# Kernel optimization log

Hardware: AMD Instinct MI355X
Metric: run time of the kernel (lower is better)

The kernel has to match this reference:

```python
import jax, jax.numpy as jnp
import numpy as np

ALPHA = 1.0

def _phi(x):
    # ELU(alpha)+1 feature map
    return jax.nn.elu(x, alpha=ALPHA) + 1.0

def setup_inputs() -> dict:
    key = jax.random.key(0)
    kq, kk, kv = jax.random.split(key, 3)
    B, H, N, D = 8, 8, 1024, 64
    Q = jax.random.normal(kq, (B, H, N, D), dtype=jnp.float32)
    K = jax.random.normal(kk, (B, H, N, D), dtype=jnp.float32)
    # NOTE: original torch code divides [.,N,dv] by [.,N,N] elementwise, so dv must equal N
    V = jax.random.normal(kv, (B, H, N, N), dtype=jnp.float32)
    return {"Q": Q, "K": K, "V": V}

def reference(Q, K, V):
    # denominator: phi(Q) @ phi(K)^T -> [B,H,N,N]
    denominator = jnp.einsum('bhnd,bhmd->bhnm', _phi(Q), _phi(K))
    # numerator: denominator @ V -> [B,H,N,N] (since dv == N)
    numerator = jnp.einsum('bhnm,bhmv->bhnv', denominator, V)
    return numerator / denominator
```

## Files before the change

kernel.cpp:

```cpp
#include <hip/hip_runtime.h>
#include <math.h>

typedef __attribute__((ext_vector_type(8))) short bf16x8;
typedef __attribute__((ext_vector_type(4))) float f32x4;
typedef __attribute__((ext_vector_type(4))) float float4v;
typedef __attribute__((ext_vector_type(2))) float float2v;
typedef __attribute__((ext_vector_type(4))) unsigned short ushort4v;

#define N_TOK 1024
#define D_DIM 64
#define BMt 128
#define BNt 128
#define BKt 32
#define KP 72
#define SP 40

__device__ __forceinline__ unsigned short f2bf(float f) {
    union { float f; unsigned u; } v; v.f = f;
    return (unsigned short)((v.u + 0x7fffu + ((v.u >> 16) & 1u)) >> 16);
}
__device__ __forceinline__ float bf2f(unsigned short h) {
    union { unsigned u; float f; } v; v.u = ((unsigned)h) << 16;
    return v.f;
}
__device__ __forceinline__ float phif(float x) {
    return x > 0.0f ? x + 1.0f : __expf(x);
}

__global__ __launch_bounds__(256)
void ka_fused(const float* __restrict__ Qp, const float* __restrict__ Kp,
              const float* __restrict__ Vp, float* __restrict__ Op)
{
    __shared__ unsigned short KhiS[32][KP], KloS[32][KP];
    __shared__ unsigned short VthiS[128][SP], VtloS[128][SP];
    __shared__ unsigned short ShiS[128][SP], SloS[128][SP];

    const int tid  = threadIdx.x;
    const int lane = tid & 63;
    const int wid  = tid >> 6;
    const int wr   = wid >> 1;
    const int wc   = wid & 1;
    const int lr   = lane & 15;
    const int lg   = lane >> 4;
    const int j0   = blockIdx.x * BNt;
    const int i0   = blockIdx.y * BMt;
    const int bh   = blockIdx.z;

    const size_t qkbase = (size_t)bh * N_TOK * D_DIM;
    const size_t vbase  = (size_t)bh * N_TOK * N_TOK;

    const f32x4 fzero = {0.f, 0.f, 0.f, 0.f};

    bf16x8 qhi[2][2], qlo[2][2];
    #pragma unroll
    for (int fr = 0; fr < 2; ++fr) {
        #pragma unroll
        for (int kb = 0; kb < 2; ++kb) {
            const float* src = Qp + qkbase
                + (size_t)(i0 + wid * 32 + fr * 16 + lr) * D_DIM + kb * 32 + lg * 8;
            float4v a = *(const float4v*)src;
            float4v b = *(const float4v*)(src + 4);
            float x[8] = {a[0], a[1], a[2], a[3], b[0], b[1], b[2], b[3]};
            bf16x8 h, l;
            #pragma unroll
            for (int e = 0; e < 8; ++e) {
                float p = phif(x[e]);
                unsigned short hh = f2bf(p);
                h[e] = (short)hh;
                l[e] = (short)f2bf(p - bf2f(hh));
            }
            qhi[fr][kb] = h;
            qlo[fr][kb] = l;
        }
    }

    f32x4 acc[4][4];
    #pragma unroll
    for (int a = 0; a < 4; ++a)
        #pragma unroll
        for (int b = 0; b < 4; ++b)
            acc[a][b] = fzero;

    for (int ms = 0; ms < N_TOK / BKt; ++ms) {
        const int m0 = ms * BKt;
        __syncthreads();

        #pragma unroll
        for (int r2 = 0; r2 < 2; ++r2) {
            int f   = tid + r2 * 256;
            int row = f >> 4;
            int dq  = (f & 15) * 4;
            float4v v = *(const float4v*)(Kp + qkbase + (size_t)(m0 + row) * D_DIM + dq);
            ushort4v h, l;
            #pragma unroll
            for (int e = 0; e < 4; ++e) {
                float p = phif(v[e]);
                h[e] = f2bf(p);
                l[e] = f2bf(p - bf2f(h[e]));
            }
            *(ushort4v*)&KhiS[row][dq] = h;
            *(ushort4v*)&KloS[row][dq] = l;
        }

        {
            int c2 = tid & 63;
            int mh = tid >> 6;
            int n  = 2 * c2;
            float va[8], vb[8];
            #pragma unroll
            for (int r = 0; r < 8; ++r) {
                float2v t = *(const float2v*)(Vp + vbase
                    + (size_t)(m0 + mh * 8 + r) * N_TOK + j0 + n);
                va[r] = t[0];
                vb[r] = t[1];
            }
            bf16x8 h, l;
            #pragma unroll
            for (int e = 0; e < 8; ++e) {
                unsigned short hh = f2bf(va[e]);
                h[e] = (short)hh;
                l[e] = (short)f2bf(va[e] - bf2f(hh));
            }
            *(bf16x8*)&VthiS[n][mh * 8] = h;
            *(bf16x8*)&VtloS[n][mh * 8] = l;
            #pragma unroll
            for (int e = 0; e < 8; ++e) {
                unsigned short hh = f2bf(vb[e]);
                h[e] = (short)hh;
                l[e] = (short)f2bf(vb[e] - bf2f(hh));
            }
            *(bf16x8*)&VthiS[n + 1][mh * 8] = h;
            *(bf16x8*)&VtloS[n + 1][mh * 8] = l;
        }
        __syncthreads();

        #pragma unroll
        for (int fr = 0; fr < 2; ++fr) {
            #pragma unroll
            for (int fc = 0; fc < 2; ++fc) {
                f32x4 sa = fzero;
                #pragma unroll
                for (int kb = 0; kb < 2; ++kb) {
                    int mcol = fc * 16 + lr;
                    int d0   = kb * 32 + lg * 8;
                    bf16x8 kh = *(const bf16x8*)&KhiS[mcol][d0];
                    bf16x8 kl = *(const bf16x8*)&KloS[mcol][d0];
                    sa = __builtin_amdgcn_mfma_f32_16x16x32_bf16(qhi[fr][kb], kh, sa, 0, 0, 0);
                    sa = __builtin_amdgcn_mfma_f32_16x16x32_bf16(qhi[fr][kb], kl, sa, 0, 0, 0);
                    sa = __builtin_amdgcn_mfma_f32_16x16x32_bf16(qlo[fr][kb], kh, sa, 0, 0, 0);
                }
                int col = fc * 16 + lr;
                int r0  = wid * 32 + fr * 16 + lg * 4;
                #pragma unroll
                for (int r = 0; r < 4; ++r) {
                    unsigned short hh = f2bf(sa[r]);
                    ShiS[r0 + r][col] = hh;
                    SloS[r0 + r][col] = f2bf(sa[r] - bf2f(hh));
                }
            }
        }
        __syncthreads();

        {
            bf16x8 sh[4], sl[4];
            int k0 = lg * 8;
            #pragma unroll
            for (int am = 0; am < 4; ++am) {
                int row = wr * 64 + am * 16 + lr;
                sh[am] = *(const bf16x8*)&ShiS[row][k0];
                sl[am] = *(const bf16x8*)&SloS[row][k0];
            }
            #pragma unroll
            for (int bn = 0; bn < 4; ++bn) {
                int col = wc * 64 + bn * 16 + lr;
                bf16x8 vh = *(const bf16x8*)&VthiS[col][k0];
                bf16x8 vl = *(const bf16x8*)&VtloS[col][k0];
                #pragma unroll
                for (int am = 0; am < 4; ++am) {
                    acc[am][bn] = __builtin_amdgcn_mfma_f32_16x16x32_bf16(sh[am], vh, acc[am][bn], 0, 0, 0);
                    acc[am][bn] = __builtin_amdgcn_mfma_f32_16x16x32_bf16(sh[am], vl, acc[am][bn], 0, 0, 0);
                    acc[am][bn] = __builtin_amdgcn_mfma_f32_16x16x32_bf16(sl[am], vh, acc[am][bn], 0, 0, 0);
                }
            }
        }
    }

    #pragma unroll
    for (int ch = 0; ch < 4; ++ch) {
        __syncthreads();
        #pragma unroll
        for (int r2 = 0; r2 < 2; ++r2) {
            int f   = tid + r2 * 256;
            int row = f >> 4;
            int dq  = (f & 15) * 4;
            float4v v = *(const float4v*)(Kp + qkbase
                + (size_t)(j0 + ch * 32 + row) * D_DIM + dq);
            ushort4v h, l;
            #pragma unroll
            for (int e = 0; e < 4; ++e) {
                float p = phif(v[e]);
                h[e] = f2bf(p);
                l[e] = f2bf(p - bf2f(h[e]));
            }
            *(ushort4v*)&KhiS[row][dq] = h;
            *(ushort4v*)&KloS[row][dq] = l;
        }
        __syncthreads();

        if (wc == (ch >> 1)) {
            const int bp = ch & 1;
            #pragma unroll
            for (int am = 0; am < 4; ++am) {
                bf16x8 qh2[2], ql2[2];
                #pragma unroll
                for (int kb = 0; kb < 2; ++kb) {
                    const float* src = Qp + qkbase
                        + (size_t)(i0 + wr * 64 + am * 16 + lr) * D_DIM + kb * 32 + lg * 8;
                    float4v a = *(const float4v*)src;
                    float4v b = *(const float4v*)(src + 4);
                    float x[8] = {a[0], a[1], a[2], a[3], b[0], b[1], b[2], b[3]};
                    bf16x8 h, l;
                    #pragma unroll
                    for (int e = 0; e < 8; ++e) {
                        float p = phif(x[e]);
                        unsigned short hh = f2bf(p);
                        h[e] = (short)hh;
                        l[e] = (short)f2bf(p - bf2f(hh));
                    }
                    qh2[kb] = h;
                    ql2[kb] = l;
                }
                #pragma unroll
                for (int fc = 0; fc < 2; ++fc) {
                    f32x4 da = fzero;
                    #pragma unroll
                    for (int kb = 0; kb < 2; ++kb) {
                        int mcol = fc * 16 + lr;
                        int d0   = kb * 32 + lg * 8;
                        bf16x8 kh = *(const bf16x8*)&KhiS[mcol][d0];
                        bf16x8 kl = *(const bf16x8*)&KloS[mcol][d0];
                        da = __builtin_amdgcn_mfma_f32_16x16x32_bf16(qh2[kb], kh, da, 0, 0, 0);
                        da = __builtin_amdgcn_mfma_f32_16x16x32_bf16(qh2[kb], kl, da, 0, 0, 0);
                        da = __builtin_amdgcn_mfma_f32_16x16x32_bf16(ql2[kb], kh, da, 0, 0, 0);
                    }
                    const int bn    = bp * 2 + fc;
                    int ocol  = j0 + wc * 64 + bn * 16 + lr;
                    int orow0 = i0 + wr * 64 + am * 16 + lg * 4;
                    #pragma unroll
                    for (int r = 0; r < 4; ++r) {
                        Op[(size_t)bh * N_TOK * N_TOK + (size_t)(orow0 + r) * N_TOK + ocol] =
                            acc[am][bn][r] / da[r];
                    }
                }
            }
        }
    }
}

extern "C" void kernel_launch(void* const* d_in, const int* in_sizes, int n_in,
                              void* d_out, int out_size, void* d_ws, size_t ws_size,
                              hipStream_t stream)
{
    const float* Q = (const float*)d_in[0];
    const float* K = (const float*)d_in[1];
    const float* V = (const float*)d_in[2];
    float* O = (float*)d_out;
    dim3 grid(N_TOK / BNt, N_TOK / BMt, 8 * 8);
    ka_fused<<<grid, 256, 0, stream>>>(Q, K, V, O);
}
```

Measured before the change: 1.291 ms.

## Drop split-bf16 low parts for phi(Q), phi(K) and V; keep split only for S

Replaces the three-term split-bf16 emulation with single bf16 for phi(Q), phi(K) and V, keeping the hi/lo split only for the intermediate S tile. This cuts MFMA count (S and denominator from 3 to 1 per k-step, PV from 3 to 2), halves LDS for K and V^T, and swaps the conversion to cheaper round-half-up packing via v_perm. It also transposes the QK^T MFMA operand order so S is written with vector stores, and remaps V load threads. The trade-off is lower accuracy in the numerator and denominator, which may exceed tolerance.

```diff
diff --git a/kernel.cpp b/kernel.cpp
--- a/kernel.cpp
+++ b/kernel.cpp
@@ -5,7 +5,8 @@
 typedef __attribute__((ext_vector_type(4))) float f32x4;
 typedef __attribute__((ext_vector_type(4))) float float4v;
 typedef __attribute__((ext_vector_type(2))) float float2v;
-typedef __attribute__((ext_vector_type(4))) unsigned short ushort4v;
+typedef __attribute__((ext_vector_type(2))) unsigned uint2v;
+typedef __attribute__((ext_vector_type(4))) unsigned uint4v;
 
 #define N_TOK 1024
 #define D_DIM 64
@@ -15,24 +16,25 @@
 #define KP 72
 #define SP 40
 
-__device__ __forceinline__ unsigned short f2bf(float f) {
-    union { float f; unsigned u; } v; v.f = f;
-    return (unsigned short)((v.u + 0x7fffu + ((v.u >> 16) & 1u)) >> 16);
-}
-__device__ __forceinline__ float bf2f(unsigned short h) {
-    union { unsigned u; float f; } v; v.u = ((unsigned)h) << 16;
-    return v.f;
-}
 __device__ __forceinline__ float phif(float x) {
     return x > 0.0f ? x + 1.0f : __expf(x);
+}
+__device__ __forceinline__ unsigned pk2(float a, float b) {
+    unsigned ua = __builtin_bit_cast(unsigned, a) + 0x8000u;
+    unsigned ub = __builtin_bit_cast(unsigned, b) + 0x8000u;
+    return __builtin_amdgcn_perm(ub, ua, 0x07060302u);
+}
+__device__ __forceinline__ unsigned pk2t(float a, float b) {
+    return __builtin_amdgcn_perm(__builtin_bit_cast(unsigned, b),
+                                 __builtin_bit_cast(unsigned, a), 0x07060302u);
 }
 
 __global__ __launch_bounds__(256)
 void ka_fused(const float* __restrict__ Qp, const float* __restrict__ Kp,
               const float* __restrict__ Vp, float* __restrict__ Op)
 {
-    __shared__ unsigned short KhiS[32][KP], KloS[32][KP];
-    __shared__ unsigned short VthiS[128][SP], VtloS[128][SP];
+    __shared__ unsigned short KhS[32][KP];
+    __shared__ unsigned short VtS[128][SP];
     __shared__ unsigned short ShiS[128][SP], SloS[128][SP];
 
     const int tid  = threadIdx.x;
@@ -48,29 +50,20 @@
 
     const size_t qkbase = (size_t)bh * N_TOK * D_DIM;
     const size_t vbase  = (size_t)bh * N_TOK * N_TOK;
-
     const f32x4 fzero = {0.f, 0.f, 0.f, 0.f};
 
-    bf16x8 qhi[2][2], qlo[2][2];
+    bf16x8 qh[2][2];
     #pragma unroll
-    for (int fr = 0; fr < 2; ++fr) {
+    for (int fc = 0; fc < 2; ++fc) {
         #pragma unroll
         for (int kb = 0; kb < 2; ++kb) {
             const float* src = Qp + qkbase
-                + (size_t)(i0 + wid * 32 + fr * 16 + lr) * D_DIM + kb * 32 + lg * 8;
+                + (size_t)(i0 + wid * 32 + fc * 16 + lr) * D_DIM + kb * 32 + lg * 8;
             float4v a = *(const float4v*)src;
             float4v b = *(const float4v*)(src + 4);
-            float x[8] = {a[0], a[1], a[2], a[3], b[0], b[1], b[2], b[3]};
-            bf16x8 h, l;
-            #pragma unroll
-            for (int e = 0; e < 8; ++e) {
-                float p = phif(x[e]);
-                unsigned short hh = f2bf(p);
-                h[e] = (short)hh;
-                l[e] = (short)f2bf(p - bf2f(hh));
-            }
-            qhi[fr][kb] = h;
-            qlo[fr][kb] = l;
+            uint4v w = { pk2(phif(a[0]), phif(a[1])), pk2(phif(a[2]), phif(a[3])),
+                         pk2(phif(b[0]), phif(b[1])), pk2(phif(b[2]), phif(b[3])) };
+            qh[fc][kb] = __builtin_bit_cast(bf16x8, w);
         }
     }
 
@@ -91,46 +84,24 @@
             int row = f >> 4;
             int dq  = (f & 15) * 4;
             float4v v = *(const float4v*)(Kp + qkbase + (size_t)(m0 + row) * D_DIM + dq);
-            ushort4v h, l;
-            #pragma unroll
-            for (int e = 0; e < 4; ++e) {
-                float p = phif(v[e]);
-                h[e] = f2bf(p);
-                l[e] = f2bf(p - bf2f(h[e]));
-            }
-            *(ushort4v*)&KhiS[row][dq] = h;
-            *(ushort4v*)&KloS[row][dq] = l;
+            uint2v w = { pk2(phif(v[0]), phif(v[1])), pk2(phif(v[2]), phif(v[3])) };
+            *(uint2v*)&KhS[row][dq] = w;
         }
 
         {
-            int c2 = tid & 63;
-            int mh = tid >> 6;
-            int n  = 2 * c2;
+            const int mh = tid & 3;
+            const int c2 = tid >> 2;
+            const float* vsrc = Vp + vbase + (size_t)(m0 + mh * 8) * N_TOK + j0 + 2 * c2;
             float va[8], vb[8];
             #pragma unroll
             for (int r = 0; r < 8; ++r) {
-                float2v t = *(const float2v*)(Vp + vbase
-                    + (size_t)(m0 + mh * 8 + r) * N_TOK + j0 + n);
-                va[r] = t[0];
-                vb[r] = t[1];
-            }
-            bf16x8 h, l;
-            #pragma unroll
-            for (int e = 0; e < 8; ++e) {
-                unsigned short hh = f2bf(va[e]);
-                h[e] = (short)hh;
-                l[e] = (short)f2bf(va[e] - bf2f(hh));
-            }
-            *(bf16x8*)&VthiS[n][mh * 8] = h;
-            *(bf16x8*)&VtloS[n][mh * 8] = l;
-            #pragma unroll
-            for (int e = 0; e < 8; ++e) {
-                unsigned short hh = f2bf(vb[e]);
-                h[e] = (short)hh;
-                l[e] = (short)f2bf(vb[e] - bf2f(hh));
-            }
-            *(bf16x8*)&VthiS[n + 1][mh * 8] = h;
-            *(bf16x8*)&VtloS[n + 1][mh * 8] = l;
+                float2v t = *(const float2v*)(vsrc + (size_t)r * N_TOK);
+                va[r] = t[0]; vb[r] = t[1];
+            }
+            uint4v wa = { pk2(va[0], va[1]), pk2(va[2], va[3]), pk2(va[4], va[5]), pk2(va[6], va[7]) };
+            uint4v wb = { pk2(vb[0], vb[1]), pk2(vb[2], vb[3]), pk2(vb[4], vb[5]), pk2(vb[6], vb[7]) };
+            *(uint4v*)&VtS[2 * c2][mh * 8]     = wa;
+            *(uint4v*)&VtS[2 * c2 + 1][mh * 8] = wb;
         }
         __syncthreads();
 
@@ -141,29 +112,31 @@
                 f32x4 sa = fzero;
                 #pragma unroll
                 for (int kb = 0; kb < 2; ++kb) {
-                    int mcol = fc * 16 + lr;
-                    int d0   = kb * 32 + lg * 8;
-                    bf16x8 kh = *(const bf16x8*)&KhiS[mcol][d0];
-                    bf16x8 kl = *(const bf16x8*)&KloS[mcol][d0];
-                    sa = __builtin_amdgcn_mfma_f32_16x16x32_bf16(qhi[fr][kb], kh, sa, 0, 0, 0);
-                    sa = __builtin_amdgcn_mfma_f32_16x16x32_bf16(qhi[fr][kb], kl, sa, 0, 0, 0);
-                    sa = __builtin_amdgcn_mfma_f32_16x16x32_bf16(qlo[fr][kb], kh, sa, 0, 0, 0);
-                }
-                int col = fc * 16 + lr;
-                int r0  = wid * 32 + fr * 16 + lg * 4;
-                #pragma unroll
-                for (int r = 0; r < 4; ++r) {
-                    unsigned short hh = f2bf(sa[r]);
-                    ShiS[r0 + r][col] = hh;
-                    SloS[r0 + r][col] = f2bf(sa[r] - bf2f(hh));
-                }
+                    bf16x8 ka = *(const bf16x8*)&KhS[fr * 16 + lr][kb * 32 + lg * 8];
+                    sa = __builtin_amdgcn_mfma_f32_16x16x32_bf16(ka, qh[fc][kb], sa, 0, 0, 0);
+                }
+                unsigned t0 = __builtin_bit_cast(unsigned, sa[0]) + 0x8000u;
+                unsigned t1 = __builtin_bit_cast(unsigned, sa[1]) + 0x8000u;
+                unsigned t2 = __builtin_bit_cast(unsigned, sa[2]) + 0x8000u;
+                unsigned t3 = __builtin_bit_cast(unsigned, sa[3]) + 0x8000u;
+                uint2v hv = { __builtin_amdgcn_perm(t1, t0, 0x07060302u),
+                              __builtin_amdgcn_perm(t3, t2, 0x07060302u) };
+                float l0 = sa[0] - __builtin_bit_cast(float, t0 & 0xffff0000u);
+                float l1 = sa[1] - __builtin_bit_cast(float, t1 & 0xffff0000u);
+                float l2 = sa[2] - __builtin_bit_cast(float, t2 & 0xffff0000u);
+                float l3 = sa[3] - __builtin_bit_cast(float, t3 & 0xffff0000u);
+                uint2v lv = { pk2t(l0, l1), pk2t(l2, l3) };
+                const int irow = wid * 32 + fc * 16 + lr;
+                const int mcol = fr * 16 + lg * 4;
+                *(uint2v*)&ShiS[irow][mcol] = hv;
+                *(uint2v*)&SloS[irow][mcol] = lv;
             }
         }
         __syncthreads();
 
         {
+            const int k0 = lg * 8;
             bf16x8 sh[4], sl[4];
-            int k0 = lg * 8;
             #pragma unroll
             for (int am = 0; am < 4; ++am) {
                 int row = wr * 64 + am * 16 + lr;
@@ -173,12 +146,10 @@
             #pragma unroll
             for (int bn = 0; bn < 4; ++bn) {
                 int col = wc * 64 + bn * 16 + lr;
-                bf16x8 vh = *(const bf16x8*)&VthiS[col][k0];
-                bf16x8 vl = *(const bf16x8*)&VtloS[col][k0];
+                bf16x8 vh = *(const bf16x8*)&VtS[col][k0];
                 #pragma unroll
                 for (int am = 0; am < 4; ++am) {
                     acc[am][bn] = __builtin_amdgcn_mfma_f32_16x16x32_bf16(sh[am], vh, acc[am][bn], 0, 0, 0);
-                    acc[am][bn] = __builtin_amdgcn_mfma_f32_16x16x32_bf16(sh[am], vl, acc[am][bn], 0, 0, 0);
                     acc[am][bn] = __builtin_amdgcn_mfma_f32_16x16x32_bf16(sl[am], vh, acc[am][bn], 0, 0, 0);
                 }
             }
@@ -195,15 +166,8 @@
             int dq  = (f & 15) * 4;
             float4v v = *(const float4v*)(Kp + qkbase
                 + (size_t)(j0 + ch * 32 + row) * D_DIM + dq);
-            ushort4v h, l;
-            #pragma unroll
-            for (int e = 0; e < 4; ++e) {
-                float p = phif(v[e]);
-                h[e] = f2bf(p);
-                l[e] = f2bf(p - bf2f(h[e]));
-            }
-            *(ushort4v*)&KhiS[row][dq] = h;
-            *(ushort4v*)&KloS[row][dq] = l;
+            uint2v w = { pk2(phif(v[0]), phif(v[1])), pk2(phif(v[2]), phif(v[3])) };
+            *(uint2v*)&KhS[row][dq] = w;
         }
         __syncthreads();
 
@@ -211,41 +175,28 @@
             const int bp = ch & 1;
             #pragma unroll
             for (int am = 0; am < 4; ++am) {
-                bf16x8 qh2[2], ql2[2];
+                bf16x8 qa[2];
                 #pragma unroll
                 for (int kb = 0; kb < 2; ++kb) {
                     const float* src = Qp + qkbase
                         + (size_t)(i0 + wr * 64 + am * 16 + lr) * D_DIM + kb * 32 + lg * 8;
                     float4v a = *(const float4v*)src;
                     float4v b = *(const float4v*)(src + 4);
-                    float x[8] = {a[0], a[1], a[2], a[3], b[0], b[1], b[2], b[3]};
-                    bf16x8 h, l;
-                    #pragma unroll
-                    for (int e = 0; e < 8; ++e) {
-                        float p = phif(x[e]);
-                        unsigned short hh = f2bf(p);
-                        h[e] = (short)hh;
-                        l[e] = (short)f2bf(p - bf2f(hh));
-                    }
-                    qh2[kb] = h;
-                    ql2[kb] = l;
+                    uint4v w = { pk2(phif(a[0]), phif(a[1])), pk2(phif(a[2]), phif(a[3])),
+                                 pk2(phif(b[0]), phif(b[1])), pk2(phif(b[2]), phif(b[3])) };
+                    qa[kb] = __builtin_bit_cast(bf16x8, w);
                 }
                 #pragma unroll
                 for (int fc = 0; fc < 2; ++fc) {
                     f32x4 da = fzero;
                     #pragma unroll
                     for (int kb = 0; kb < 2; ++kb) {
-                        int mcol = fc * 16 + lr;
-                        int d0   = kb * 32 + lg * 8;
-                        bf16x8 kh = *(const bf16x8*)&KhiS[mcol][d0];
-                        bf16x8 kl = *(const bf16x8*)&KloS[mcol][d0];
-                        da = __builtin_amdgcn_mfma_f32_16x16x32_bf16(qh2[kb], kh, da, 0, 0, 0);
-                        da = __builtin_amdgcn_mfma_f32_16x16x32_bf16(qh2[kb], kl, da, 0, 0, 0);
-                        da = __builtin_amdgcn_mfma_f32_16x16x32_bf16(ql2[kb], kh, da, 0, 0, 0);
+                        bf16x8 kB = *(const bf16x8*)&KhS[fc * 16 + lr][kb * 32 + lg * 8];
+                        da = __builtin_amdgcn_mfma_f32_16x16x32_bf16(qa[kb], kB, da, 0, 0, 0);
                     }
                     const int bn    = bp * 2 + fc;
-                    int ocol  = j0 + wc * 64 + bn * 16 + lr;
-                    int orow0 = i0 + wr * 64 + am * 16 + lg * 4;
+                    const int ocol  = j0 + wc * 64 + bn * 16 + lr;
+                    const int orow0 = i0 + wr * 64 + am * 16 + lg * 4;
                     #pragma unroll
                     for (int r = 0; r < 4; ++r) {
                         Op[(size_t)bh * N_TOK * N_TOK + (size_t)(orow0 + r) * N_TOK + ocol] =
```

New measurement: 1.116 ms. 1.16x faster.
